# Performance work log

Measured on AMD Instinct MI355X. Metric: run time of the kernel, lower is better.

The kernel has to match this reference:

```python
import jax, jax.numpy as jnp
import numpy as np

N = 50000          # nodes
E = 1_600_000      # edges
IN = 256           # in_channels
C = 32             # hidden_channels (per-head width)
HEADS = 4
BN_EPS = 1e-5


def setup_inputs() -> dict:
    key = jax.random.key(0)
    ks = jax.random.split(key, 32)
    g = lambda k, shp, s=0.1: (jax.random.normal(k, shp, jnp.float32) * s)
    inp = {
        "x": jax.random.normal(ks[0], (N, IN), jnp.float32),
        "edge_index": jax.random.randint(ks[1], (2, E), 0, N, jnp.int64),
        "edge_attr": jax.random.uniform(ks[2], (E, 1), jnp.float32),
        # conv1 (GATConv in=IN, out=C, heads=HEADS, edge_dim=1)
        "W1": g(ks[3], (IN, HEADS * C)),
        "as1": g(ks[4], (HEADS, C)),
        "ad1": g(ks[5], (HEADS, C)),
        "We1": g(ks[6], (1, HEADS * C)),
        "ae1": g(ks[7], (HEADS, C)),
        "b1": jnp.zeros((HEADS * C,), jnp.float32),
        # bn1 (eval mode, running_mean=0, running_var=1)
        "g1": jnp.ones((HEADS * C,), jnp.float32),
        "be1": jnp.zeros((HEADS * C,), jnp.float32),
        # conv2 (GATConv in=HEADS*C, out=C, heads=1, concat=False, edge_dim=1)
        "W2": g(ks[8], (HEADS * C, C)),
        "as2": g(ks[9], (1, C)),
        "ad2": g(ks[10], (1, C)),
        "We2": g(ks[11], (1, C)),
        "ae2": g(ks[12], (1, C)),
        "b2": jnp.zeros((C,), jnp.float32),
        # bn2
        "g2": jnp.ones((C,), jnp.float32),
        "be2": jnp.zeros((C,), jnp.float32),
        # classifier: Linear(C,16) -> ReLU -> Linear(16,2)
        "Wc1": g(ks[13], (C, 16)),
        "bc1": jnp.zeros((16,), jnp.float32),
        "Wc2": g(ks[14], (16, 2)),
        "bc2": jnp.zeros((2,), jnp.float32),
        "Wr1": g(ks[15], (C, 16)),
        "br1": jnp.zeros((16,), jnp.float32),
        "Wr2": g(ks[16], (16, 1)),
        "br2": jnp.zeros((1,), jnp.float32),
    }
    return inp


def _gat_conv(x, src, dst, eattr, W, a_src, a_dst, We, a_e, bias, heads, c, concat):
    n = x.shape[0]
    xs = (x @ W).reshape(n, heads, c)                       # [N,H,C]
    al_s = (xs * a_src).sum(-1)                              # [N,H]
    al_d = (xs * a_dst).sum(-1)                              # [N,H]
    ee = (eattr @ We).reshape(-1, heads, c)                  # [E,H,C]
    al_e = (ee * a_e).sum(-1)                                # [E,H]
    alpha = al_s[src] + al_d[dst] + al_e                     # [E,H]
    alpha = jax.nn.leaky_relu(alpha, 0.2)
    # segment softmax over destination node
    mx = jax.ops.segment_max(alpha, dst, num_segments=n)
    ex = jnp.exp(alpha - mx[dst])
    den = jax.ops.segment_sum(ex, dst, num_segments=n)
    a = ex / (den[dst] + 1e-16)                              # [E,H]
    out = jax.ops.segment_sum(xs[src] * a[..., None], dst, num_segments=n)  # [N,H,C]
    out = out.reshape(n, heads * c) if concat else out.mean(axis=1)
    return out + bias


def _add_self_loops(src, dst, eattr, n):
    loop = jnp.arange(n, dtype=src.dtype)
    fill = jnp.broadcast_to(eattr.mean(axis=0, keepdims=True), (n, eattr.shape[1]))
    return (jnp.concatenate([src, loop]), jnp.concatenate([dst, loop]),
            jnp.concatenate([eattr, fill], axis=0))


def _bn_eval(x, gamma, beta):
    # running_mean=0, running_var=1 (fresh BatchNorm1d, eval mode)
    return x * (gamma / jnp.sqrt(1.0 + BN_EPS)) + beta


def reference(x, edge_index, edge_attr, W1, as1, ad1, We1, ae1, b1, g1, be1,
              W2, as2, ad2, We2, ae2, b2, g2, be2,
              Wc1, bc1, Wc2, bc2, Wr1, br1, Wr2, br2):
    n = x.shape[0]
    src, dst, ea = _add_self_loops(edge_index[0], edge_index[1], edge_attr, n)
    h = _gat_conv(x, src, dst, ea, W1, as1, ad1, We1, ae1, b1, HEADS, C, True)
    h = jax.nn.elu(_bn_eval(h, g1, be1))
    h = _gat_conv(h, src, dst, ea, W2, as2, ad2, We2, ae2, b2, 1, C, False)
    h = jax.nn.elu(_bn_eval(h, g2, be2))
    cls = jax.nn.relu(h @ Wc1 + bc1) @ Wc2 + bc2             # [N,2]
    reg = (jax.nn.relu(h @ Wr1 + br1) @ Wr2 + br2)[:, 0]     # [N]
    return cls, reg, h
```

## Files before the change

kernel.cpp:

```cpp
#include <hip/hip_runtime.h>
#include <cstdint>
#include <cstddef>

#define NN 50000
#define EE 1600000
#define IN_DIM 256
#define HC 128
#define CD 32
#define BN_RS 0.9999950000374997f

#define CAP1 120
#define CAP2 128
#define NBKT 196
#define S1_B 782
#define HIST_B 320
#define G1_B 782

typedef __attribute__((ext_vector_type(8))) short short8;
typedef __attribute__((ext_vector_type(4))) float f32x4;

__device__ __forceinline__ float lrelu(float a) { return a > 0.f ? a : 0.2f * a; }
__device__ __forceinline__ float elu(float a) { return a > 0.f ? a : (__expf(a) - 1.f); }

__device__ __forceinline__ unsigned short f2bf(float f) {
    unsigned int u = __float_as_uint(f);
    unsigned int r = (u + 0x7FFFu + ((u >> 16) & 1u)) >> 16;
    return (unsigned short)r;
}
__device__ __forceinline__ float bf2f(unsigned short b) {
    return __uint_as_float(((unsigned int)b) << 16);
}
__device__ __forceinline__ float2 bf2f2(unsigned int p) {
    float2 r;
    r.x = __uint_as_float(p << 16);
    r.y = __uint_as_float(p & 0xFFFF0000u);
    return r;
}
__device__ __forceinline__ void unpack_edge(unsigned long long p, int& s, float& eav) {
    s = (int)(unsigned int)(p & 0xFFFFFFFFull);
    eav = __uint_as_float((unsigned int)(p >> 32));
}
__device__ __forceinline__ float pick4(float a, float b, float c, float d, int h) {
    return (h & 2) ? ((h & 1) ? d : c) : ((h & 1) ? b : a);
}

__device__ __forceinline__ int block_excl_scan_256(int v, int tid, int* wsum) {
    int lane = tid & 63, wv = tid >> 6;
    int x = v;
    #pragma unroll
    for (int off = 1; off < 64; off <<= 1) {
        int y = __shfl_up(x, off);
        if (lane >= off) x += y;
    }
    if (lane == 63) wsum[wv] = x;
    __syncthreads();
    int wpre = 0;
    #pragma unroll
    for (int w = 0; w < 4; w++)
        if (w < wv) wpre += wsum[w];
    return wpre + x - v;
}

__global__ __launch_bounds__(256) void k0_prep(const float* __restrict__ W1,
                                               const float* __restrict__ W2,
                                               const float* __restrict__ We1,
                                               const float* __restrict__ ae1,
                                               const float* __restrict__ We2,
                                               const float* __restrict__ ae2,
                                               unsigned short* __restrict__ W1hi,
                                               unsigned short* __restrict__ W1lo,
                                               unsigned short* __restrict__ W2hi,
                                               unsigned short* __restrict__ W2lo,
                                               float* __restrict__ consts,
                                               int* __restrict__ bucketHist) {
    int blk = blockIdx.x;
    int tid = threadIdx.x;
    if (blk < 16) {
        int t = blk * 256 + tid;
        int lane = t & 63;
        int kt = (t >> 6) & 7;
        int nt = t >> 9;
        int kbase = kt * 32 + (lane >> 4) * 8;
        int col = nt * 16 + (lane & 15);
        size_t obase = (size_t)t * 8;
        #pragma unroll
        for (int j = 0; j < 8; j++) {
            float w = W1[(size_t)(kbase + j) * HC + col];
            unsigned short h = f2bf(w);
            W1hi[obase + j] = h;
            W1lo[obase + j] = f2bf(w - bf2f(h));
        }
    } else if (blk < 18) {
        int t = (blk - 16) * 256 + tid;
        int lane = t & 63;
        int kt = (t >> 6) & 3;
        int nt = t >> 8;
        int kbase = kt * 32 + (lane >> 4) * 8;
        int col = nt * 16 + (lane & 15);
        size_t obase = (size_t)t * 8;
        #pragma unroll
        for (int j = 0; j < 8; j++) {
            float w = W2[(size_t)(kbase + j) * CD + col];
            unsigned short h = f2bf(w);
            W2hi[obase + j] = h;
            W2lo[obase + j] = f2bf(w - bf2f(h));
        }
    } else {
        if (tid < NBKT) bucketHist[tid] = 0;
        if (tid == 200) consts[0] = 0.f;
        if (tid < 4) {
            float s = 0.f;
            for (int c = 0; c < 32; c++) s += We1[tid * 32 + c] * ae1[tid * 32 + c];
            consts[2 + tid] = s;
        } else if (tid == 4) {
            float s = 0.f;
            for (int c = 0; c < 32; c++) s += We2[c] * ae2[c];
            consts[6] = s;
        }
    }
}

__global__ __launch_bounds__(256) void kA_hist_gemm1(const int* __restrict__ ei,
                                                     const float* __restrict__ ea,
                                                     const float* __restrict__ x,
                                                     const unsigned short* __restrict__ Whi,
                                                     const unsigned short* __restrict__ Wlo,
                                                     int* __restrict__ bucketHist,
                                                     float* __restrict__ easum,
                                                     unsigned short* __restrict__ xs1b) {
    __shared__ int h[256];
    int tid = threadIdx.x;
    if (blockIdx.x < HIST_B) {
        h[tid] = 0;
        __syncthreads();
        float s = 0.f;
        for (int i = blockIdx.x * 256 + tid; i < EE; i += HIST_B * 256) {
            atomicAdd(&h[ei[EE + i] >> 8], 1);
            s += ea[i];
        }
        __syncthreads();
        if (tid < NBKT && h[tid] > 0) atomicAdd(&bucketHist[tid], h[tid]);
        #pragma unroll
        for (int off = 32; off > 0; off >>= 1) s += __shfl_xor(s, off);
        if ((tid & 63) == 0) atomicAdd(easum, s);
    } else {
        int lane = tid & 63, wv = tid >> 6;
        int row0 = (blockIdx.x - HIST_B) * 64 + wv * 16;
        if (row0 >= NN) return;
        int m = lane & 15;
        int q = lane >> 4;
        f32x4 acc[8];
        #pragma unroll
        for (int nt = 0; nt < 8; nt++) acc[nt] = {0.f, 0.f, 0.f, 0.f};
        const float* xrow = x + (size_t)(row0 + m) * IN_DIM + q * 8;
        #pragma unroll
        for (int kt = 0; kt < 8; kt++) {
            float4 v0 = *(const float4*)(xrow + kt * 32);
            float4 v1 = *(const float4*)(xrow + kt * 32 + 4);
            float vv[8] = {v0.x, v0.y, v0.z, v0.w, v1.x, v1.y, v1.z, v1.w};
            short8 ahi, alo;
            #pragma unroll
            for (int j = 0; j < 8; j++) {
                unsigned short hh = f2bf(vv[j]);
                ahi[j] = (short)hh;
                alo[j] = (short)f2bf(vv[j] - bf2f(hh));
            }
            #pragma unroll
            for (int nt = 0; nt < 8; nt++) {
                size_t fb = ((size_t)(nt * 8 + kt) * 64 + lane) * 8;
                short8 bhi = *(const short8*)(Whi + fb);
                short8 blo = *(const short8*)(Wlo + fb);
                acc[nt] = __builtin_amdgcn_mfma_f32_16x16x32_bf16(ahi, bhi, acc[nt], 0, 0, 0);
                acc[nt] = __builtin_amdgcn_mfma_f32_16x16x32_bf16(ahi, blo, acc[nt], 0, 0, 0);
                acc[nt] = __builtin_amdgcn_mfma_f32_16x16x32_bf16(alo, bhi, acc[nt], 0, 0, 0);
            }
        }
        #pragma unroll
        for (int nt = 0; nt < 8; nt++) {
            #pragma unroll
            for (int reg = 0; reg < 4; reg++) {
                int row = row0 + q * 4 + reg;
                xs1b[(size_t)row * HC + nt * 16 + m] = f2bf(acc[nt][reg]);
            }
        }
    }
}

__global__ void bucket_scan(const int* __restrict__ bucketHist,
                            int* __restrict__ bucketBase,
                            int* __restrict__ bucketCursor,
                            int* __restrict__ indptr,
                            float* __restrict__ consts) {
    __shared__ int wsum[4];
    int tid = threadIdx.x;
    int v = (tid < NBKT) ? bucketHist[tid] : 0;
    int excl = block_excl_scan_256(v, tid, wsum);
    if (tid <= NBKT) bucketBase[tid] = (tid == NBKT) ? EE : excl;
    if (tid < NBKT) bucketCursor[tid] = excl;
    if (tid == 0) { indptr[NN] = EE; consts[1] = consts[0] / (float)EE; }
}

__global__ __launch_bounds__(256) void kB_stage1_al1(const int* __restrict__ ei,
                                                     const float* __restrict__ ea,
                                                     int* __restrict__ bucketCursor,
                                                     int* __restrict__ Adst,
                                                     int* __restrict__ Asrc,
                                                     float* __restrict__ Aea,
                                                     const unsigned short* __restrict__ xs1b,
                                                     const float* __restrict__ as1,
                                                     const float* __restrict__ ad1,
                                                     float* __restrict__ als,
                                                     float* __restrict__ ald) {
    __shared__ int cnt[256];
    __shared__ int basel[256];
    __shared__ int gbase[256];
    __shared__ int wsum[4];
    __shared__ int sdst[2048];
    __shared__ int ssrc[2048];
    __shared__ float sea[2048];
    int tid = threadIdx.x;
    if (blockIdx.x < S1_B) {
        int base = blockIdx.x * 2048;
        cnt[tid] = 0;
        __syncthreads();
        int d[8], s[8], r[8], bk[8];
        float e[8];
        #pragma unroll
        for (int k = 0; k < 8; k++) {
            int i = base + k * 256 + tid;
            if (i < EE) {
                d[k] = ei[EE + i];
                s[k] = ei[i];
                e[k] = ea[i];
                bk[k] = d[k] >> 8;
                r[k] = atomicAdd(&cnt[bk[k]], 1);
            } else d[k] = -1;
        }
        __syncthreads();
        int v = cnt[tid];
        int excl = block_excl_scan_256(v, tid, wsum);
        basel[tid] = excl;
        if (tid < NBKT) gbase[tid] = atomicAdd(&bucketCursor[tid], v);
        __syncthreads();
        #pragma unroll
        for (int k = 0; k < 8; k++) {
            if (d[k] >= 0) {
                int slot = basel[bk[k]] + r[k];
                sdst[slot] = d[k];
                ssrc[slot] = s[k];
                sea[slot] = e[k];
            }
        }
        __syncthreads();
        int total = basel[255] + cnt[255];
        for (int slot = tid; slot < total; slot += 256) {
            int dd = sdst[slot];
            int b = dd >> 8;
            int pos = gbase[b] + (slot - basel[b]);
            Adst[pos] = dd;
            Asrc[pos] = ssrc[slot];
            Aea[pos] = sea[slot];
        }
    } else {
        int t = (blockIdx.x - S1_B) * 256 + tid;
        if (t < NN * 4) {
            int hh = t & 3;
            const unsigned int* xp = (const unsigned int*)(xs1b + (size_t)t * 32);
            const float* ap = as1 + hh * 32;
            const float* dp = ad1 + hh * 32;
            float s = 0.f, d = 0.f;
            #pragma unroll
            for (int q = 0; q < 16; q++) {
                float2 v = bf2f2(xp[q]);
                s += v.x * ap[q * 2] + v.y * ap[q * 2 + 1];
                d += v.x * dp[q * 2] + v.y * dp[q * 2 + 1];
            }
            als[t] = s;
            ald[t] = d;
        }
    }
}

__global__ __launch_bounds__(1024) void stage2_kernel(const int* __restrict__ bucketBase,
                                                      const int* __restrict__ Adst,
                                                      const int* __restrict__ Asrc,
                                                      const float* __restrict__ Aea,
                                                      int* __restrict__ indptr,
                                                      unsigned long long* __restrict__ edgedat) {
    __shared__ int cnt[256];
    __shared__ int dbase[256];
    int tid = threadIdx.x;
    int b = blockIdx.x;
    int start = bucketBase[b], end = bucketBase[b + 1];
    if (tid < 256) cnt[tid] = 0;
    __syncthreads();
    for (int i = start + tid; i < end; i += 1024) atomicAdd(&cnt[Adst[i] & 255], 1);
    __syncthreads();
    if (tid < 64) {
        int b4 = tid * 4;
        int c0 = cnt[b4], c1 = cnt[b4 + 1], c2 = cnt[b4 + 2], c3 = cnt[b4 + 3];
        int t = c0 + c1 + c2 + c3;
        int x = t;
        #pragma unroll
        for (int off = 1; off < 64; off <<= 1) {
            int y = __shfl_up(x, off);
            if (tid >= off) x += y;
        }
        int e0 = x - t;
        dbase[b4] = e0;
        dbase[b4 + 1] = e0 + c0;
        dbase[b4 + 2] = e0 + c0 + c1;
        dbase[b4 + 3] = e0 + c0 + c1 + c2;
    }
    __syncthreads();
    if (tid < 256) {
        int n = b * 256 + tid;
        if (n < NN) indptr[n] = start + dbase[tid];
        cnt[tid] = 0;
    }
    __syncthreads();
    for (int i = start + tid; i < end; i += 1024) {
        int dl = Adst[i] & 255;
        int r = atomicAdd(&cnt[dl], 1);
        int pos = start + dbase[dl] + r;
        edgedat[pos] = (unsigned long long)(unsigned int)Asrc[i] |
                       ((unsigned long long)__float_as_uint(Aea[i]) << 32);
    }
}

#define ACC4(vv, ww) { float2 p0_ = bf2f2((vv).x); float2 p1_ = bf2f2((vv).y); \
    acc0 += p0_.x * (ww); acc1 += p0_.y * (ww); acc2 += p1_.x * (ww); acc3 += p1_.y * (ww); }

__global__ __launch_bounds__(256, 8) void gat1_agg(
    const unsigned short* __restrict__ xs1b, const float* __restrict__ als,
    const float* __restrict__ ald, const unsigned long long* __restrict__ edgedat,
    const int* __restrict__ indptr, const float* __restrict__ consts,
    const float* __restrict__ b1, const float* __restrict__ g1,
    const float* __restrict__ be1,
    unsigned short* __restrict__ h1hi, unsigned short* __restrict__ h1lo) {
    __shared__ __align__(16) float exbuf[8][CAP1][4];
    __shared__ int srcbuf[8][CAP1];
    int tid = threadIdx.x;
    int l = tid & 31;
    int nb = tid >> 5;
    int n = blockIdx.x * 8 + nb;
    int start = indptr[n];
    int deg = indptr[n + 1] - start;
    float ea_mean = consts[1];
    float ce0 = consts[2], ce1 = consts[3], ce2 = consts[4], ce3 = consts[5];
    float4 a4d = *(const float4*)(ald + (size_t)n * 4);
    float4 a4s = *(const float4*)(als + (size_t)n * 4);
    float ex00 = __expf(lrelu(a4s.x + a4d.x + ea_mean * ce0));
    float ex01 = __expf(lrelu(a4s.y + a4d.y + ea_mean * ce1));
    float ex02 = __expf(lrelu(a4s.z + a4d.z + ea_mean * ce2));
    float ex03 = __expf(lrelu(a4s.w + a4d.w + ea_mean * ce3));
    float sm0 = 0.f, sm1 = 0.f, sm2 = 0.f, sm3 = 0.f;
    const unsigned long long* edp = edgedat + start;
    for (int i = l; i < deg; i += 32) {
        int s; float eav;
        unpack_edge(edp[i], s, eav);
        float4 v4 = *(const float4*)(als + (size_t)s * 4);
        float4 ex4;
        ex4.x = __expf(lrelu(v4.x + a4d.x + eav * ce0)); sm0 += ex4.x;
        ex4.y = __expf(lrelu(v4.y + a4d.y + eav * ce1)); sm1 += ex4.y;
        ex4.z = __expf(lrelu(v4.z + a4d.z + eav * ce2)); sm2 += ex4.z;
        ex4.w = __expf(lrelu(v4.w + a4d.w + eav * ce3)); sm3 += ex4.w;
        if (i < CAP1) {
            srcbuf[nb][i] = s * (HC * 2);
            *(float4*)(&exbuf[nb][i][0]) = ex4;
        }
    }
    #pragma unroll
    for (int off = 16; off > 0; off >>= 1) {
        sm0 += __shfl_xor(sm0, off);
        sm1 += __shfl_xor(sm1, off);
        sm2 += __shfl_xor(sm2, off);
        sm3 += __shfl_xor(sm3, off);
    }
    int h2 = l >> 3;
    float ex0sel = pick4(ex00, ex01, ex02, ex03, h2);
    float inv = 1.0f / (pick4(sm0, sm1, sm2, sm3, h2) + ex0sel + 1e-16f);
    int mcap = deg < CAP1 ? deg : CAP1;
    const char* xb = (const char*)xs1b + (size_t)l * 8;
    float acc0, acc1, acc2, acc3;
    {
        uint2 v = *(const uint2*)(xb + (size_t)n * (HC * 2));
        float2 p0 = bf2f2(v.x), p1 = bf2f2(v.y);
        acc0 = p0.x * ex0sel; acc1 = p0.y * ex0sel;
        acc2 = p1.x * ex0sel; acc3 = p1.y * ex0sel;
    }
    int i = 0;
    for (; i + 8 <= mcap; i += 8) {
        int o0 = srcbuf[nb][i + 0], o1 = srcbuf[nb][i + 1];
        int o2 = srcbuf[nb][i + 2], o3 = srcbuf[nb][i + 3];
        int o4 = srcbuf[nb][i + 4], o5 = srcbuf[nb][i + 5];
        int o6 = srcbuf[nb][i + 6], o7 = srcbuf[nb][i + 7];
        float w0 = exbuf[nb][i + 0][h2], w1 = exbuf[nb][i + 1][h2];
        float w2 = exbuf[nb][i + 2][h2], w3 = exbuf[nb][i + 3][h2];
        float w4 = exbuf[nb][i + 4][h2], w5 = exbuf[nb][i + 5][h2];
        float w6 = exbuf[nb][i + 6][h2], w7 = exbuf[nb][i + 7][h2];
        uint2 v0 = *(const uint2*)(xb + o0);
        uint2 v1 = *(const uint2*)(xb + o1);
        uint2 v2 = *(const uint2*)(xb + o2);
        uint2 v3 = *(const uint2*)(xb + o3);
        uint2 v4 = *(const uint2*)(xb + o4);
        uint2 v5 = *(const uint2*)(xb + o5);
        uint2 v6 = *(const uint2*)(xb + o6);
        uint2 v7 = *(const uint2*)(xb + o7);
        ACC4(v0, w0); ACC4(v1, w1); ACC4(v2, w2); ACC4(v3, w3);
        ACC4(v4, w4); ACC4(v5, w5); ACC4(v6, w6); ACC4(v7, w7);
    }
    for (; i < mcap; i++) {
        int o = srcbuf[nb][i];
        float w = exbuf[nb][i][h2];
        uint2 v = *(const uint2*)(xb + o);
        ACC4(v, w);
    }
    if (deg > CAP1) {
        float aldsel = pick4(a4d.x, a4d.y, a4d.z, a4d.w, h2);
        float cesel = pick4(ce0, ce1, ce2, ce3, h2);
        for (int j = CAP1; j < deg; j++) {
            int s; float eav;
            unpack_edge(edp[j], s, eav);
            float w = __expf(lrelu(als[(size_t)s * 4 + h2] + aldsel + eav * cesel));
            uint2 v = *(const uint2*)(xb + (size_t)s * (HC * 2));
            ACC4(v, w);
        }
    }
    acc0 *= inv; acc1 *= inv; acc2 *= inv; acc3 *= inv;
    int c = l * 4;
    float4 bb = *(const float4*)(b1 + c);
    float4 gg = *(const float4*)(g1 + c);
    float4 eb = *(const float4*)(be1 + c);
    float o0 = elu((acc0 + bb.x) * (gg.x * BN_RS) + eb.x);
    float o1 = elu((acc1 + bb.y) * (gg.y * BN_RS) + eb.y);
    float o2 = elu((acc2 + bb.z) * (gg.z * BN_RS) + eb.z);
    float o3 = elu((acc3 + bb.w) * (gg.w * BN_RS) + eb.w);
    unsigned short h0 = f2bf(o0), h1v = f2bf(o1), h2v = f2bf(o2), h3v = f2bf(o3);
    unsigned short l0 = f2bf(o0 - bf2f(h0)), l1 = f2bf(o1 - bf2f(h1v));
    unsigned short l2 = f2bf(o2 - bf2f(h2v)), l3 = f2bf(o3 - bf2f(h3v));
    uint2 hiw, low;
    hiw.x = (unsigned int)h0 | ((unsigned int)h1v << 16);
    hiw.y = (unsigned int)h2v | ((unsigned int)h3v << 16);
    low.x = (unsigned int)l0 | ((unsigned int)l1 << 16);
    low.y = (unsigned int)l2 | ((unsigned int)l3 << 16);
    *(uint2*)(h1hi + (size_t)n * HC + c) = hiw;
    *(uint2*)(h1lo + (size_t)n * HC + c) = low;
}

__global__ __launch_bounds__(256) void gemm2_mfma(const unsigned short* __restrict__ h1hi,
                                                  const unsigned short* __restrict__ h1lo,
                                                  const unsigned short* __restrict__ W2hi,
                                                  const unsigned short* __restrict__ W2lo,
                                                  const float* __restrict__ as2,
                                                  const float* __restrict__ ad2,
                                                  unsigned short* __restrict__ xs2b,
                                                  float* __restrict__ als2,
                                                  float* __restrict__ ald2) {
    int tid = threadIdx.x;
    int lane = tid & 63, wv = tid >> 6;
    int row0 = blockIdx.x * 64 + wv * 16;
    if (row0 >= NN) return;
    int m = lane & 15, q = lane >> 4;
    f32x4 acc[2];
    acc[0] = {0.f, 0.f, 0.f, 0.f};
    acc[1] = {0.f, 0.f, 0.f, 0.f};
    const unsigned short* rhi = h1hi + (size_t)(row0 + m) * HC + q * 8;
    const unsigned short* rlo = h1lo + (size_t)(row0 + m) * HC + q * 8;
    #pragma unroll
    for (int kt = 0; kt < 4; kt++) {
        short8 ahi = *(const short8*)(rhi + kt * 32);
        short8 alo = *(const short8*)(rlo + kt * 32);
        #pragma unroll
        for (int nt = 0; nt < 2; nt++) {
            size_t fb = ((size_t)(nt * 4 + kt) * 64 + lane) * 8;
            short8 bhi = *(const short8*)(W2hi + fb);
            short8 blo = *(const short8*)(W2lo + fb);
            acc[nt] = __builtin_amdgcn_mfma_f32_16x16x32_bf16(ahi, bhi, acc[nt], 0, 0, 0);
            acc[nt] = __builtin_amdgcn_mfma_f32_16x16x32_bf16(ahi, blo, acc[nt], 0, 0, 0);
            acc[nt] = __builtin_amdgcn_mfma_f32_16x16x32_bf16(alo, bhi, acc[nt], 0, 0, 0);
        }
    }
    float a0 = as2[m], a1 = as2[m + 16];
    float d0 = ad2[m], d1 = ad2[m + 16];
    #pragma unroll
    for (int reg = 0; reg < 4; reg++) {
        int row = row0 + q * 4 + reg;
        xs2b[(size_t)row * CD + m]      = f2bf(acc[0][reg]);
        xs2b[(size_t)row * CD + 16 + m] = f2bf(acc[1][reg]);
        float s = acc[0][reg] * a0 + acc[1][reg] * a1;
        float d = acc[0][reg] * d0 + acc[1][reg] * d1;
        #pragma unroll
        for (int off = 1; off < 16; off <<= 1) {
            s += __shfl_xor(s, off);
            d += __shfl_xor(d, off);
        }
        if (m == 0) { als2[row] = s; ald2[row] = d; }
    }
}

__global__ __launch_bounds__(256) void gat2_agg(
    const unsigned short* __restrict__ xs2b, const float* __restrict__ als,
    const float* __restrict__ ald, const unsigned long long* __restrict__ edgedat,
    const int* __restrict__ indptr, const float* __restrict__ consts,
    const float* __restrict__ b2, const float* __restrict__ g2, const float* __restrict__ be2,
    const float* __restrict__ Wc1, const float* __restrict__ bc1,
    const float* __restrict__ Wc2, const float* __restrict__ bc2,
    const float* __restrict__ Wr1, const float* __restrict__ br1,
    const float* __restrict__ Wr2, const float* __restrict__ br2,
    float* __restrict__ hout, float* __restrict__ cls, float* __restrict__ reg) {
    __shared__ float exbuf[4][CAP2];
    __shared__ int srcbuf[4][CAP2];
    __shared__ __align__(16) float hbuf[4][32];
    int wv = threadIdx.x >> 6;
    int lane = threadIdx.x & 63;
    int n = blockIdx.x * 4 + wv;
    int start = indptr[n];
    int deg = indptr[n + 1] - start;
    float ea_mean = consts[1];
    float ce = consts[6];
    float aldn = ald[n];
    float ex0 = __expf(lrelu(als[n] + aldn + ea_mean * ce));
    float sm = 0.f;
    const unsigned long long* edp = edgedat + start;
    for (int i = lane; i < deg; i += 64) {
        int s; float eav;
        unpack_edge(edp[i], s, eav);
        float exv = __expf(lrelu(als[s] + aldn + eav * ce));
        if (i < CAP2) { srcbuf[wv][i] = s * (CD * 2); exbuf[wv][i] = exv; }
        sm += exv;
    }
    #pragma unroll
    for (int off = 32; off > 0; off >>= 1) sm += __shfl_xor(sm, off);
    float invd = 1.0f / (sm + ex0 + 1e-16f);
    int mcap = deg < CAP2 ? deg : CAP2;
    int oct = lane >> 3, lo = lane & 7;
    const char* xb = (const char*)xs2b + (size_t)lo * 8;
    float acc0 = 0.f, acc1 = 0.f, acc2 = 0.f, acc3 = 0.f;
    if (oct == 0) {
        uint2 v = *(const uint2*)(xb + (size_t)n * (CD * 2));
        float2 p0 = bf2f2(v.x), p1 = bf2f2(v.y);
        acc0 = p0.x * ex0; acc1 = p0.y * ex0; acc2 = p1.x * ex0; acc3 = p1.y * ex0;
    }
    for (int i = oct; i < mcap; i += 8) {
        float w = exbuf[wv][i];
        int o = srcbuf[wv][i];
        uint2 v = *(const uint2*)(xb + o);
        ACC4(v, w);
    }
    for (int i = CAP2 + oct; i < deg; i += 8) {
        int s; float eav;
        unpack_edge(edp[i], s, eav);
        float w = __expf(lrelu(als[s] + aldn + eav * ce));
        uint2 v = *(const uint2*)(xb + (size_t)s * (CD * 2));
        ACC4(v, w);
    }
    #pragma unroll
    for (int off = 8; off < 64; off <<= 1) {
        acc0 += __shfl_xor(acc0, off);
        acc1 += __shfl_xor(acc1, off);
        acc2 += __shfl_xor(acc2, off);
        acc3 += __shfl_xor(acc3, off);
    }
    if (lane < 8) {
        int c = lo * 4;
        float4 bb = *(const float4*)(b2 + c);
        float4 gg = *(const float4*)(g2 + c);
        float4 eb = *(const float4*)(be2 + c);
        float o0 = elu((acc0 * invd + bb.x) * (gg.x * BN_RS) + eb.x);
        float o1 = elu((acc1 * invd + bb.y) * (gg.y * BN_RS) + eb.y);
        float o2 = elu((acc2 * invd + bb.z) * (gg.z * BN_RS) + eb.z);
        float o3 = elu((acc3 * invd + bb.w) * (gg.w * BN_RS) + eb.w);
        *(float4*)(&hbuf[wv][c]) = make_float4(o0, o1, o2, o3);
        *(float4*)(hout + (size_t)n * CD + c) = make_float4(o0, o1, o2, o3);
    }
    float r0 = 0.f, r1 = 0.f;
    if (lane < 32) {
        int j = lane & 15;
        bool iscls = lane < 16;
        float s = iscls ? bc1[j] : br1[j];
        #pragma unroll
        for (int cc = 0; cc < 32; cc++) {
            float w = iscls ? Wc1[cc * 16 + j] : Wr1[cc * 16 + j];
            s += hbuf[wv][cc] * w;
        }
        s = fmaxf(s, 0.f);
        if (iscls) { r0 = s * Wc2[j * 2]; r1 = s * Wc2[j * 2 + 1]; }
        else       { r0 = s * Wr2[j]; }
    }
    #pragma unroll
    for (int off = 1; off < 16; off <<= 1) {
        r0 += __shfl_xor(r0, off);
        r1 += __shfl_xor(r1, off);
    }
    if (lane == 0)  *(float2*)(cls + (size_t)n * 2) = make_float2(r0 + bc2[0], r1 + bc2[1]);
    if (lane == 16) reg[n] = r0 + br2[0];
}

extern "C" void kernel_launch(void* const* d_in, const int* in_sizes, int n_in,
                              void* d_out, int out_size, void* d_ws, size_t ws_size,
                              hipStream_t stream) {
    const float* x   = (const float*)d_in[0];
    const int*   ei  = (const int*)d_in[1];
    const float* ea  = (const float*)d_in[2];
    const float* W1  = (const float*)d_in[3];
    const float* as1 = (const float*)d_in[4];
    const float* ad1 = (const float*)d_in[5];
    const float* We1 = (const float*)d_in[6];
    const float* ae1 = (const float*)d_in[7];
    const float* b1  = (const float*)d_in[8];
    const float* g1  = (const float*)d_in[9];
    const float* be1 = (const float*)d_in[10];
    const float* W2  = (const float*)d_in[11];
    const float* as2 = (const float*)d_in[12];
    const float* ad2 = (const float*)d_in[13];
    const float* We2 = (const float*)d_in[14];
    const float* ae2 = (const float*)d_in[15];
    const float* b2  = (const float*)d_in[16];
    const float* g2  = (const float*)d_in[17];
    const float* be2 = (const float*)d_in[18];
    const float* Wc1 = (const float*)d_in[19];
    const float* bc1 = (const float*)d_in[20];
    const float* Wc2 = (const float*)d_in[21];
    const float* bc2 = (const float*)d_in[22];
    const float* Wr1 = (const float*)d_in[23];
    const float* br1 = (const float*)d_in[24];
    const float* Wr2 = (const float*)d_in[25];
    const float* br2 = (const float*)d_in[26];

    char* ws = (char*)d_ws;
    unsigned short* xs1b = (unsigned short*)(ws + 0);
    unsigned short* h1hi = (unsigned short*)(ws + 12800000);
    unsigned short* h1lo = (unsigned short*)(ws + 25600000);
    int*   Adst          = (int*)(ws + 12800000);
    int*   Asrc          = (int*)(ws + 19200000);
    float* Aea           = (float*)(ws + 25600000);
    unsigned short* xs2b = (unsigned short*)(ws + 38400000);
    float* als1          = (float*)(ws + 41600000);
    float* ald1          = (float*)(ws + 42400000);
    float* als2          = (float*)(ws + 43200000);
    float* ald2          = (float*)(ws + 43400000);
    float* consts        = (float*)(ws + 43600000);
    int*   bucketHist    = (int*)(ws + 43600128);
    int*   bucketBase    = (int*)(ws + 43601024);
    int*   bucketCursor  = (int*)(ws + 43601920);
    int*   indptr        = (int*)(ws + 43602816);
    unsigned long long* edgedat = (unsigned long long*)(ws + 43802824);
    unsigned short* W1hi = (unsigned short*)(ws + 56602832);
    unsigned short* W1lo = (unsigned short*)(ws + 56668368);
    unsigned short* W2hi = (unsigned short*)(ws + 56733904);
    unsigned short* W2lo = (unsigned short*)(ws + 56742096);

    float* out_cls = (float*)d_out;
    float* out_reg = out_cls + 2 * NN;
    float* out_h   = out_cls + 3 * NN;

    k0_prep<<<19, 256, 0, stream>>>(W1, W2, We1, ae1, We2, ae2,
                                    W1hi, W1lo, W2hi, W2lo, consts, bucketHist);
    kA_hist_gemm1<<<HIST_B + G1_B, 256, 0, stream>>>(ei, ea, x, W1hi, W1lo,
                                                     bucketHist, consts, xs1b);
    bucket_scan<<<1, 256, 0, stream>>>(bucketHist, bucketBase, bucketCursor, indptr, consts);
    kB_stage1_al1<<<S1_B + 782, 256, 0, stream>>>(ei, ea, bucketCursor, Adst, Asrc, Aea,
                                                  xs1b, as1, ad1, als1, ald1);
    stage2_kernel<<<NBKT, 1024, 0, stream>>>(bucketBase, Adst, Asrc, Aea, indptr, edgedat);

    gat1_agg<<<NN / 8, 256, 0, stream>>>(xs1b, als1, ald1, edgedat, indptr, consts,
                                         b1, g1, be1, h1hi, h1lo);
    gemm2_mfma<<<G1_B, 256, 0, stream>>>(h1hi, h1lo, W2hi, W2lo, as2, ad2,
                                         xs2b, als2, ald2);
    gat2_agg<<<NN / 4, 256, 0, stream>>>(xs2b, als2, ald2, edgedat, indptr, consts,
                                         b2, g2, be2, Wc1, bc1, Wc2, bc2,
                                         Wr1, br1, Wr2, br2, out_h, out_cls, out_reg);
}
```

Baseline: 340.1 us.

## Bucket-sort per-node neighbor lists by source range before gather in gat1_agg

Each warp counts its cached edges into 7 source-index tiles (src>>13) with shared atomics, prefix-sums the counts, then rewrites srcbuf in tile order. The packed offset keeps the original edge slot in its low 8 bits so the matching attention weight can still be found. The goal is to make concurrent gathers from xs1b hit nearby rows and so improve L2 locality. In exchange it adds three block-wide __syncthreads, shared-memory atomics and extra bit masking per edge, and edge summation order changes.

```diff
diff --git a/kernel.cpp b/kernel.cpp
--- a/kernel.cpp
+++ b/kernel.cpp
@@ -15,6 +15,9 @@
 #define S1_B 782
 #define HIST_B 320
 #define G1_B 782
+
+#define NT1 7
+#define TSH 13
 
 typedef __attribute__((ext_vector_type(8))) short short8;
 typedef __attribute__((ext_vector_type(4))) float f32x4;
@@ -340,12 +343,15 @@
     unsigned short* __restrict__ h1hi, unsigned short* __restrict__ h1lo) {
     __shared__ __align__(16) float exbuf[8][CAP1][4];
     __shared__ int srcbuf[8][CAP1];
+    __shared__ int tcnt[8][8];
+    __shared__ int tbase[8][8];
     int tid = threadIdx.x;
     int l = tid & 31;
     int nb = tid >> 5;
     int n = blockIdx.x * 8 + nb;
     int start = indptr[n];
     int deg = indptr[n + 1] - start;
+    if (l < 8) tcnt[nb][l] = 0;
     float ea_mean = consts[1];
     float ce0 = consts[2], ce1 = consts[3], ce2 = consts[4], ce3 = consts[5];
     float4 a4d = *(const float4*)(ald + (size_t)n * 4);
@@ -356,19 +362,34 @@
     float ex03 = __expf(lrelu(a4s.w + a4d.w + ea_mean * ce3));
     float sm0 = 0.f, sm1 = 0.f, sm2 = 0.f, sm3 = 0.f;
     const unsigned long long* edp = edgedat + start;
-    for (int i = l; i < deg; i += 32) {
-        int s; float eav;
-        unpack_edge(edp[i], s, eav);
-        float4 v4 = *(const float4*)(als + (size_t)s * 4);
-        float4 ex4;
-        ex4.x = __expf(lrelu(v4.x + a4d.x + eav * ce0)); sm0 += ex4.x;
-        ex4.y = __expf(lrelu(v4.y + a4d.y + eav * ce1)); sm1 += ex4.y;
-        ex4.z = __expf(lrelu(v4.z + a4d.z + eav * ce2)); sm2 += ex4.z;
-        ex4.w = __expf(lrelu(v4.w + a4d.w + eav * ce3)); sm3 += ex4.w;
-        if (i < CAP1) {
-            srcbuf[nb][i] = s * (HC * 2);
-            *(float4*)(&exbuf[nb][i][0]) = ex4;
-        }
+    int mcap = deg < CAP1 ? deg : CAP1;
+    __syncthreads();
+
+    int s0v = -1, s1v = -1, s2v = -1, s3v = -1;
+#define P1STEP(K, SV) { int i = l + 32 * K; if (i < deg) { \
+        int s_; float eav_; unpack_edge(edp[i], s_, eav_); \
+        float4 v4_ = *(const float4*)(als + (size_t)s_ * 4); \
+        float4 ex4_; \
+        ex4_.x = __expf(lrelu(v4_.x + a4d.x + eav_ * ce0)); sm0 += ex4_.x; \
+        ex4_.y = __expf(lrelu(v4_.y + a4d.y + eav_ * ce1)); sm1 += ex4_.y; \
+        ex4_.z = __expf(lrelu(v4_.z + a4d.z + eav_ * ce2)); sm2 += ex4_.z; \
+        ex4_.w = __expf(lrelu(v4_.w + a4d.w + eav_ * ce3)); sm3 += ex4_.w; \
+        if (i < CAP1) { SV = s_; \
+            *(float4*)(&exbuf[nb][i][0]) = ex4_; \
+            atomicAdd(&tcnt[nb][s_ >> TSH], 1); } } }
+    P1STEP(0, s0v)
+    P1STEP(1, s1v)
+    P1STEP(2, s2v)
+    P1STEP(3, s3v)
+#undef P1STEP
+    for (int i = l + 128; i < deg; i += 32) {
+        int s_; float eav_;
+        unpack_edge(edp[i], s_, eav_);
+        float4 v4_ = *(const float4*)(als + (size_t)s_ * 4);
+        sm0 += __expf(lrelu(v4_.x + a4d.x + eav_ * ce0));
+        sm1 += __expf(lrelu(v4_.y + a4d.y + eav_ * ce1));
+        sm2 += __expf(lrelu(v4_.z + a4d.z + eav_ * ce2));
+        sm3 += __expf(lrelu(v4_.w + a4d.w + eav_ * ce3));
     }
     #pragma unroll
     for (int off = 16; off > 0; off >>= 1) {
@@ -377,10 +398,26 @@
         sm2 += __shfl_xor(sm2, off);
         sm3 += __shfl_xor(sm3, off);
     }
+    __syncthreads();
+    if (l == 0) {
+        int a_ = 0;
+        #pragma unroll
+        for (int t = 0; t < NT1; t++) { int c_ = tcnt[nb][t]; tbase[nb][t] = a_; a_ += c_; }
+    }
+    __syncthreads();
+#define P1PLACE(K, SV) { if (SV >= 0) { int t_ = SV >> TSH; \
+        int slot_ = atomicAdd(&tbase[nb][t_], 1); \
+        srcbuf[nb][slot_] = SV * (HC * 2) + (l + 32 * K); } }
+    P1PLACE(0, s0v)
+    P1PLACE(1, s1v)
+    P1PLACE(2, s2v)
+    P1PLACE(3, s3v)
+#undef P1PLACE
+    __syncthreads();
+
     int h2 = l >> 3;
     float ex0sel = pick4(ex00, ex01, ex02, ex03, h2);
     float inv = 1.0f / (pick4(sm0, sm1, sm2, sm3, h2) + ex0sel + 1e-16f);
-    int mcap = deg < CAP1 ? deg : CAP1;
     const char* xb = (const char*)xs1b + (size_t)l * 8;
     float acc0, acc1, acc2, acc3;
     {
@@ -391,29 +428,29 @@
     }
     int i = 0;
     for (; i + 8 <= mcap; i += 8) {
-        int o0 = srcbuf[nb][i + 0], o1 = srcbuf[nb][i + 1];
-        int o2 = srcbuf[nb][i + 2], o3 = srcbuf[nb][i + 3];
-        int o4 = srcbuf[nb][i + 4], o5 = srcbuf[nb][i + 5];
-        int o6 = srcbuf[nb][i + 6], o7 = srcbuf[nb][i + 7];
-        float w0 = exbuf[nb][i + 0][h2], w1 = exbuf[nb][i + 1][h2];
-        float w2 = exbuf[nb][i + 2][h2], w3 = exbuf[nb][i + 3][h2];
-        float w4 = exbuf[nb][i + 4][h2], w5 = exbuf[nb][i + 5][h2];
-        float w6 = exbuf[nb][i + 6][h2], w7 = exbuf[nb][i + 7][h2];
-        uint2 v0 = *(const uint2*)(xb + o0);
-        uint2 v1 = *(const uint2*)(xb + o1);
-        uint2 v2 = *(const uint2*)(xb + o2);
-        uint2 v3 = *(const uint2*)(xb + o3);
-        uint2 v4 = *(const uint2*)(xb + o4);
-        uint2 v5 = *(const uint2*)(xb + o5);
-        uint2 v6 = *(const uint2*)(xb + o6);
-        uint2 v7 = *(const uint2*)(xb + o7);
+        int q0 = srcbuf[nb][i + 0], q1 = srcbuf[nb][i + 1];
+        int q2 = srcbuf[nb][i + 2], q3 = srcbuf[nb][i + 3];
+        int q4 = srcbuf[nb][i + 4], q5 = srcbuf[nb][i + 5];
+        int q6 = srcbuf[nb][i + 6], q7 = srcbuf[nb][i + 7];
+        float w0 = exbuf[nb][q0 & 255][h2], w1 = exbuf[nb][q1 & 255][h2];
+        float w2 = exbuf[nb][q2 & 255][h2], w3 = exbuf[nb][q3 & 255][h2];
+        float w4 = exbuf[nb][q4 & 255][h2], w5 = exbuf[nb][q5 & 255][h2];
+        float w6 = exbuf[nb][q6 & 255][h2], w7 = exbuf[nb][q7 & 255][h2];
+        uint2 v0 = *(const uint2*)(xb + (q0 & 0x7FFFFF00));
+        uint2 v1 = *(const uint2*)(xb + (q1 & 0x7FFFFF00));
+        uint2 v2 = *(const uint2*)(xb + (q2 & 0x7FFFFF00));
+        uint2 v3 = *(const uint2*)(xb + (q3 & 0x7FFFFF00));
+        uint2 v4 = *(const uint2*)(xb + (q4 & 0x7FFFFF00));
+        uint2 v5 = *(const uint2*)(xb + (q5 & 0x7FFFFF00));
+        uint2 v6 = *(const uint2*)(xb + (q6 & 0x7FFFFF00));
+        uint2 v7 = *(const uint2*)(xb + (q7 & 0x7FFFFF00));
         ACC4(v0, w0); ACC4(v1, w1); ACC4(v2, w2); ACC4(v3, w3);
         ACC4(v4, w4); ACC4(v5, w5); ACC4(v6, w6); ACC4(v7, w7);
     }
     for (; i < mcap; i++) {
-        int o = srcbuf[nb][i];
-        float w = exbuf[nb][i][h2];
-        uint2 v = *(const uint2*)(xb + o);
+        int q = srcbuf[nb][i];
+        float w = exbuf[nb][q & 255][h2];
+        uint2 v = *(const uint2*)(xb + (q & 0x7FFFFF00));
         ACC4(v, w);
     }
     if (deg > CAP1) {
```

Measured after the change: 343.1 us. Within noise of the previous version (+0.9%).
